# Performance work log

Hardware: AMD Instinct MI355X
Metric: run time of the kernel (lower is better)

## Reference

```python
import jax, jax.numpy as jnp
import numpy as np

H, W, L = 512, 512, 28
N_ITER = 12
SIGMA = 0.5
LAM = 1.0
PI = 3.141592653589793


def _offsets(s, phi_deg):
    # Matches torch: dx = s*cos(phi), dy = s*sin(phi), shifted to min 0, round-half-even.
    phi = phi_deg * PI / 180.0
    dx = s * np.cos(phi)
    dy = s * np.sin(phi)
    dx = dx - dx.min()
    dy = dy - dy.min()
    return np.rint(dx).astype(np.int32), np.rint(dy).astype(np.int32)


def _gauss_kernel(sigma):
    ksize = max(3, int(6 * sigma + 1) | 1)  # 5 for sigma=0.5
    ax = np.arange(ksize, dtype=np.float32) - ksize // 2
    g1 = np.exp(-0.5 * (ax / sigma) ** 2)
    g1 = g1 / g1.sum()
    g2 = np.outer(g1, g1).astype(np.float32)
    return jnp.asarray(g2)[None, None], ksize // 2  # [1,1,k,k], pad


def setup_inputs():
    k1, k2 = jax.random.split(jax.random.key(0))
    s_nom = jnp.arange(L, dtype=jnp.float32)
    phi_d_deg = jnp.ones((), dtype=jnp.float32)
    dx, dy = _offsets(np.arange(L, dtype=np.float32), 1.0)
    Hp, Wp = H + int(dy.max()), W + int(dx.max())
    y_1hw = jax.random.uniform(k1, (1, Hp, Wp), dtype=jnp.float32)
    mask2d = jax.random.uniform(k2, (H, W), dtype=jnp.float32)
    return {"y_1hw": y_1hw, "mask2d": mask2d, "phi_d_deg": phi_d_deg, "s_nom": s_nom}


def reference(y_1hw, mask2d, phi_d_deg, s_nom):
    # Integer dispersion offsets are detached (.item()) in the original, so they
    # are compile-time constants here.
    dx, dy = _offsets(np.asarray(s_nom), float(np.asarray(phi_d_deg)))
    Hp, Wp = H + int(dy.max()), W + int(dx.max())
    rows = dy[:, None, None] + np.arange(H, dtype=np.int64)[None, :, None]  # [L,H,1]
    cols = dx[:, None, None] + np.arange(W, dtype=np.int64)[None, None, :]  # [L,1,W]
    flat = jnp.asarray(rows * Wp + cols)  # [L,H,W] flat indices into [Hp*Wp]

    g2, pad = _gauss_kernel(SIGMA)

    def A(x):  # CASSI forward: [L,H,W] -> [Hp,Wp] batched scatter-add
        return jnp.zeros(Hp * Wp, x.dtype).at[flat].add(mask2d[None] * x).reshape(Hp, Wp)

    def At(y2):  # CASSI adjoint: [Hp,Wp] -> [L,H,W] batched gather
        return y2.reshape(-1)[flat] * mask2d[None]

    def denoise(x):  # depthwise 5x5 Gaussian; same 2D kernel per band -> bands as batch
        return jax.lax.conv_general_dilated(
            x[:, None], g2, (1, 1), [(pad, pad), (pad, pad)])[:, 0]

    # Phi_sum = sum over bands of shifted mask, clamped to >= 1
    Phi_sum = jnp.maximum(
        jnp.zeros(Hp * Wp, mask2d.dtype).at[flat].add(
            jnp.broadcast_to(mask2d[None], (L, H, W))).reshape(Hp, Wp),
        1.0)

    y = y_1hw[0]
    x = At(y)   # adjoint back-projection initialization
    y1 = y
    for _ in range(N_ITER):  # unrolled GAP iterations (accelerated GAP)
        yb = A(x)
        y1 = y1 + (y - yb)
        x = x + LAM * At((y1 - yb) / Phi_sum)
        x = denoise(x)
    return x[None]  # [1, L, H, W]
```

## Files before the change

kernel.cpp:

```cpp
#include <hip/hip_runtime.h>

#define HH 512
#define WW 512
#define LL 28
#define WP 539
#define NPIX (HH * WP)
#define NX (LL * HH * WW)

#define TX 64
#define TY 16
#define GB 7
#define NGRP (LL / GB)

__global__ void k_setup(const float* __restrict__ y, const float* __restrict__ mask,
                        float* __restrict__ phi_inv, float* __restrict__ y1) {
    int idx = blockIdx.x * blockDim.x + threadIdx.x;
    if (idx >= NPIX) return;
    int i = idx / WP, jp = idx - i * WP;
    int lmin = jp - (WW - 1); if (lmin < 0) lmin = 0;
    int lmax = jp < (LL - 1) ? jp : (LL - 1);
    float s = 0.f;
    for (int l = lmin; l <= lmax; ++l) s += mask[i * WW + (jp - l)];
    phi_inv[idx] = 1.0f / fmaxf(s, 1.0f);
    y1[idx] = y[idx];
}

__global__ void k_xinit(const float* __restrict__ y, const float* __restrict__ mask,
                        float* __restrict__ x, float* __restrict__ yb) {
    __shared__ float ybl[TY][TX + GB - 1];
    const int l0 = blockIdx.z * GB;
    const int bi = blockIdx.y * TY;
    const int bj = blockIdx.x * TX;
    const int tid = threadIdx.x;

    for (int idx = tid; idx < TY * (TX + GB - 1); idx += 256)
        ybl[idx / (TX + GB - 1)][idx % (TX + GB - 1)] = 0.f;
    __syncthreads();

    for (int l = l0; l < l0 + GB; ++l) {
        #pragma unroll
        for (int k = 0; k < 4; ++k) {
            int idx = tid + k * 256;
            int r = idx / TX, c = idx - r * TX;
            int gi = bi + r, gj = bj + c;
            float m = mask[gi * WW + gj];
            float v = y[gi * WP + gj + l] * m;
            x[((size_t)l * HH + gi) * WW + gj] = v;
            ybl[r][c + (l - l0)] += m * v;
        }
        __syncthreads();
    }
    for (int idx = tid; idx < TY * (TX + GB - 1); idx += 256) {
        int r = idx / (TX + GB - 1), c = idx % (TX + GB - 1);
        atomicAdd(&yb[(bi + r) * WP + bj + l0 + c], ybl[r][c]);
    }
}

__global__ void k_pix(const float* __restrict__ y, const float* __restrict__ phi_inv,
                      float* __restrict__ y1, float* __restrict__ t, float* __restrict__ yb) {
    int idx = blockIdx.x * blockDim.x + threadIdx.x;
    if (idx >= NPIX / 4) return;
    float4 ybv = ((const float4*)yb)[idx];
    float4 yv  = ((const float4*)y)[idx];
    float4 y1v = ((const float4*)y1)[idx];
    float4 pv  = ((const float4*)phi_inv)[idx];
    float4 y1n, tv;
    y1n.x = y1v.x + yv.x - ybv.x;  tv.x = (y1n.x - ybv.x) * pv.x;
    y1n.y = y1v.y + yv.y - ybv.y;  tv.y = (y1n.y - ybv.y) * pv.y;
    y1n.z = y1v.z + yv.z - ybv.z;  tv.z = (y1n.z - ybv.z) * pv.z;
    y1n.w = y1v.w + yv.w - ybv.w;  tv.w = (y1n.w - ybv.w) * pv.w;
    ((float4*)y1)[idx] = y1n;
    ((float4*)t)[idx]  = tv;
    ((float4*)yb)[idx] = make_float4(0.f, 0.f, 0.f, 0.f);
}

template <bool LAST>
__global__ void k_iter(const float* __restrict__ x, const float* __restrict__ t,
                       const float* __restrict__ mask, float* __restrict__ xo,
                       float* __restrict__ yb, float w0, float w1, float w2) {
    __shared__ float msk[TY + 4][TX + 4];
    __shared__ float u[TY + 4][TX + 4];
    __shared__ float hb[TY + 4][TX];
    __shared__ float ybl[TY][TX + GB - 1];

    const int l0 = blockIdx.z * GB;
    const int bi = blockIdx.y * TY;
    const int bj = blockIdx.x * TX;
    const int tid = threadIdx.x;

    for (int idx = tid; idx < (TY + 4) * (TX + 4); idx += 256) {
        int r = idx / (TX + 4), c = idx - r * (TX + 4);
        int gi = bi + r - 2, gj = bj + c - 2;
        msk[r][c] = (gi >= 0 && gi < HH && gj >= 0 && gj < WW) ? mask[gi * WW + gj] : 0.f;
    }
    if (!LAST)
        for (int idx = tid; idx < TY * (TX + GB - 1); idx += 256)
            ybl[idx / (TX + GB - 1)][idx % (TX + GB - 1)] = 0.f;
    __syncthreads();

    for (int l = l0; l < l0 + GB; ++l) {
        const float* xl = x + (size_t)l * HH * WW;
        for (int idx = tid; idx < (TY + 4) * (TX + 4); idx += 256) {
            int r = idx / (TX + 4), c = idx - r * (TX + 4);
            int gi = bi + r - 2, gj = bj + c - 2;
            float v = 0.f;
            if (gi >= 0 && gi < HH && gj >= 0 && gj < WW)
                v = xl[gi * WW + gj] + t[gi * WP + gj + l] * msk[r][c];
            u[r][c] = v;
        }
        __syncthreads();
        for (int idx = tid; idx < (TY + 4) * TX; idx += 256) {
            int r = idx / TX, c = idx - r * TX;
            hb[r][c] = w2 * (u[r][c] + u[r][c + 4])
                     + w1 * (u[r][c + 1] + u[r][c + 3])
                     + w0 * u[r][c + 2];
        }
        __syncthreads();
        #pragma unroll
        for (int k = 0; k < 4; ++k) {
            int idx = tid + k * 256;
            int r = idx / TX, c = idx - r * TX;
            float o = w2 * (hb[r][c] + hb[r + 4][c])
                    + w1 * (hb[r + 1][c] + hb[r + 3][c])
                    + w0 * hb[r + 2][c];
            xo[((size_t)l * HH + bi + r) * WW + bj + c] = o;
            if (!LAST) ybl[r][c + (l - l0)] += msk[r + 2][c + 2] * o;
        }
        __syncthreads();
    }

    if (!LAST)
        for (int idx = tid; idx < TY * (TX + GB - 1); idx += 256) {
            int r = idx / (TX + GB - 1), c = idx % (TX + GB - 1);
            atomicAdd(&yb[(bi + r) * WP + bj + l0 + c], ybl[r][c]);
        }
}

extern "C" void kernel_launch(void* const* d_in, const int* in_sizes, int n_in,
                              void* d_out, int out_size, void* d_ws, size_t ws_size,
                              hipStream_t stream) {
    const float* y    = (const float*)d_in[0];
    const float* mask = (const float*)d_in[1];

    float* out = (float*)d_out;

    float* phi_inv = (float*)d_ws;
    float* y1      = phi_inv + NPIX;
    float* t       = y1 + NPIX;
    float* yb      = t + NPIX;
    float* xA      = yb + NPIX;
    float* xB      = out;

    float g1 = expf(-2.0f), g2 = expf(-8.0f);
    float gs = 1.0f + 2.0f * g1 + 2.0f * g2;
    float w0 = 1.0f / gs, w1 = g1 / gs, w2 = g2 / gs;

    const int BT = 256;
    const dim3 tgrid(WW / TX, HH / TY, NGRP);

    hipMemsetAsync(yb, 0, NPIX * sizeof(float), stream);
    k_setup<<<(NPIX + BT - 1) / BT, BT, 0, stream>>>(y, mask, phi_inv, y1);
    k_xinit<<<tgrid, BT, 0, stream>>>(y, mask, xB, yb);

    float* cur = xB;
    float* nxt = xA;
    for (int it = 0; it < 12; ++it) {
        k_pix<<<(NPIX / 4 + BT - 1) / BT, BT, 0, stream>>>(y, phi_inv, y1, t, yb);
        if (it < 11)
            k_iter<false><<<tgrid, BT, 0, stream>>>(cur, t, mask, nxt, yb, w0, w1, w2);
        else
            k_iter<true><<<tgrid, BT, 0, stream>>>(cur, t, mask, nxt, yb, w0, w1, w2);
        float* tmp = cur; cur = nxt; nxt = tmp;
    }
}
```

Before: 484.1 us.

## Stage t tile once per band group in LDS and simplify tile indexing

Loads the shifted t halo tile once per block into shared memory, covering all bands in the group, instead of re-reading t from global memory for every band. It replaces the div/mod index loops with fixed 2D thread mapping (tx,ty) and a separate bounds-check-free fast path for interior tiles. It also adds launch bounds and uses fma. This cuts global traffic and integer overhead at the cost of extra LDS usage and more code.

Result: slower. 550.1 us (+13.6%).

```diff
diff --git a/kernel.cpp b/kernel.cpp
--- a/kernel.cpp
+++ b/kernel.cpp
@@ -25,38 +25,45 @@
     y1[idx] = y[idx];
 }
 
-__global__ void k_xinit(const float* __restrict__ y, const float* __restrict__ mask,
+__global__ __launch_bounds__(256) void k_xinit(const float* __restrict__ y, const float* __restrict__ mask,
                         float* __restrict__ x, float* __restrict__ yb) {
     __shared__ float ybl[TY][TX + GB - 1];
     const int l0 = blockIdx.z * GB;
     const int bi = blockIdx.y * TY;
     const int bj = blockIdx.x * TX;
     const int tid = threadIdx.x;
-
-    for (int idx = tid; idx < TY * (TX + GB - 1); idx += 256)
-        ybl[idx / (TX + GB - 1)][idx % (TX + GB - 1)] = 0.f;
+    const int tx = tid & 63;
+    const int ty = tid >> 6;
+
+    #pragma unroll
+    for (int k = 0; k < 4; ++k) {
+        int r = ty + 4 * k;
+        ybl[r][tx] = 0.f;
+        if (tx < GB - 1) ybl[r][64 + tx] = 0.f;
+    }
     __syncthreads();
 
     for (int l = l0; l < l0 + GB; ++l) {
         #pragma unroll
         for (int k = 0; k < 4; ++k) {
-            int idx = tid + k * 256;
-            int r = idx / TX, c = idx - r * TX;
-            int gi = bi + r, gj = bj + c;
+            int r = ty + 4 * k;
+            int gi = bi + r, gj = bj + tx;
             float m = mask[gi * WW + gj];
             float v = y[gi * WP + gj + l] * m;
             x[((size_t)l * HH + gi) * WW + gj] = v;
-            ybl[r][c + (l - l0)] += m * v;
-        }
-        __syncthreads();
-    }
-    for (int idx = tid; idx < TY * (TX + GB - 1); idx += 256) {
-        int r = idx / (TX + GB - 1), c = idx % (TX + GB - 1);
-        atomicAdd(&yb[(bi + r) * WP + bj + l0 + c], ybl[r][c]);
-    }
-}
-
-__global__ void k_pix(const float* __restrict__ y, const float* __restrict__ phi_inv,
+            ybl[r][tx + (l - l0)] += m * v;
+        }
+        __syncthreads();
+    }
+    #pragma unroll
+    for (int k = 0; k < 4; ++k) {
+        int r = ty + 4 * k;
+        atomicAdd(&yb[(bi + r) * WP + bj + l0 + tx], ybl[r][tx]);
+        if (tx < GB - 1) atomicAdd(&yb[(bi + r) * WP + bj + l0 + 64 + tx], ybl[r][64 + tx]);
+    }
+}
+
+__global__ __launch_bounds__(256) void k_pix(const float* __restrict__ y, const float* __restrict__ phi_inv,
                       float* __restrict__ y1, float* __restrict__ t, float* __restrict__ yb) {
     int idx = blockIdx.x * blockDim.x + threadIdx.x;
     if (idx >= NPIX / 4) return;
@@ -75,10 +82,11 @@
 }
 
 template <bool LAST>
-__global__ void k_iter(const float* __restrict__ x, const float* __restrict__ t,
+__global__ __launch_bounds__(256) void k_iter(const float* __restrict__ x, const float* __restrict__ t,
                        const float* __restrict__ mask, float* __restrict__ xo,
                        float* __restrict__ yb, float w0, float w1, float w2) {
     __shared__ float msk[TY + 4][TX + 4];
+    __shared__ float tld[TY + 4][TX + 4 + GB - 1];
     __shared__ float u[TY + 4][TX + 4];
     __shared__ float hb[TY + 4][TX];
     __shared__ float ybl[TY][TX + GB - 1];
@@ -87,53 +95,106 @@
     const int bi = blockIdx.y * TY;
     const int bj = blockIdx.x * TX;
     const int tid = threadIdx.x;
-
-    for (int idx = tid; idx < (TY + 4) * (TX + 4); idx += 256) {
-        int r = idx / (TX + 4), c = idx - r * (TX + 4);
-        int gi = bi + r - 2, gj = bj + c - 2;
-        msk[r][c] = (gi >= 0 && gi < HH && gj >= 0 && gj < WW) ? mask[gi * WW + gj] : 0.f;
-    }
-    if (!LAST)
-        for (int idx = tid; idx < TY * (TX + GB - 1); idx += 256)
-            ybl[idx / (TX + GB - 1)][idx % (TX + GB - 1)] = 0.f;
+    const int tx = tid & 63;
+    const int ty = tid >> 6;
+    const bool edge = (bi == 0) | (bi == HH - TY) | (bj == 0) | (bj == WW - TX);
+
+    #pragma unroll
+    for (int k = 0; k < 5; ++k) {
+        int r = ty + 4 * k;
+        int gi = bi + r - 2;
+        bool rok = (gi >= 0) & (gi < HH);
+        int gj0 = bj + tx - 2;
+        float m0 = 0.f;
+        if (rok & (gj0 >= 0) & (gj0 < WW)) m0 = mask[gi * WW + gj0];
+        msk[r][tx] = m0;
+        if (tx < 4) {
+            int gj1 = bj + 64 + tx - 2;
+            float m1 = 0.f;
+            if (rok & (gj1 < WW)) m1 = mask[gi * WW + gj1];
+            msk[r][64 + tx] = m1;
+        }
+        int tg0 = bj - 2 + l0 + tx;
+        float v0 = 0.f;
+        if (rok & (tg0 >= 0) & (tg0 < WP)) v0 = t[gi * WP + tg0];
+        tld[r][tx] = v0;
+        if (tx < 4 + GB - 1) {
+            int tg1 = tg0 + 64;
+            float v1 = 0.f;
+            if (rok & (tg1 < WP)) v1 = t[gi * WP + tg1];
+            tld[r][64 + tx] = v1;
+        }
+    }
+    if (!LAST) {
+        #pragma unroll
+        for (int k = 0; k < 4; ++k) {
+            int r = ty + 4 * k;
+            ybl[r][tx] = 0.f;
+            if (tx < GB - 1) ybl[r][64 + tx] = 0.f;
+        }
+    }
     __syncthreads();
 
     for (int l = l0; l < l0 + GB; ++l) {
         const float* xl = x + (size_t)l * HH * WW;
-        for (int idx = tid; idx < (TY + 4) * (TX + 4); idx += 256) {
-            int r = idx / (TX + 4), c = idx - r * (TX + 4);
-            int gi = bi + r - 2, gj = bj + c - 2;
-            float v = 0.f;
-            if (gi >= 0 && gi < HH && gj >= 0 && gj < WW)
-                v = xl[gi * WW + gj] + t[gi * WP + gj + l] * msk[r][c];
-            u[r][c] = v;
-        }
-        __syncthreads();
-        for (int idx = tid; idx < (TY + 4) * TX; idx += 256) {
-            int r = idx / TX, c = idx - r * TX;
-            hb[r][c] = w2 * (u[r][c] + u[r][c + 4])
-                     + w1 * (u[r][c + 1] + u[r][c + 3])
-                     + w0 * u[r][c + 2];
-        }
-        __syncthreads();
-        #pragma unroll
-        for (int k = 0; k < 4; ++k) {
-            int idx = tid + k * 256;
-            int r = idx / TX, c = idx - r * TX;
-            float o = w2 * (hb[r][c] + hb[r + 4][c])
-                    + w1 * (hb[r + 1][c] + hb[r + 3][c])
-                    + w0 * hb[r + 2][c];
-            xo[((size_t)l * HH + bi + r) * WW + bj + c] = o;
-            if (!LAST) ybl[r][c + (l - l0)] += msk[r + 2][c + 2] * o;
-        }
-        __syncthreads();
-    }
-
-    if (!LAST)
-        for (int idx = tid; idx < TY * (TX + GB - 1); idx += 256) {
-            int r = idx / (TX + GB - 1), c = idx % (TX + GB - 1);
-            atomicAdd(&yb[(bi + r) * WP + bj + l0 + c], ybl[r][c]);
-        }
+        const int dl = l - l0;
+        if (!edge) {
+            #pragma unroll
+            for (int k = 0; k < 5; ++k) {
+                int r = ty + 4 * k;
+                const float* xrow = xl + (bi + r - 2) * WW + bj - 2;
+                u[r][tx] = fmaf(tld[r][tx + dl], msk[r][tx], xrow[tx]);
+                if (tx < 4) u[r][64 + tx] = fmaf(tld[r][64 + tx + dl], msk[r][64 + tx], xrow[64 + tx]);
+            }
+        } else {
+            #pragma unroll
+            for (int k = 0; k < 5; ++k) {
+                int r = ty + 4 * k;
+                int gi = bi + r - 2;
+                bool rok = (gi >= 0) & (gi < HH);
+                int gj0 = bj + tx - 2;
+                float v0 = 0.f;
+                if (rok & (gj0 >= 0) & (gj0 < WW))
+                    v0 = fmaf(tld[r][tx + dl], msk[r][tx], xl[gi * WW + gj0]);
+                u[r][tx] = v0;
+                if (tx < 4) {
+                    int gj1 = bj + 64 + tx - 2;
+                    float v1 = 0.f;
+                    if (rok & (gj1 < WW))
+                        v1 = fmaf(tld[r][64 + tx + dl], msk[r][64 + tx], xl[gi * WW + gj1]);
+                    u[r][64 + tx] = v1;
+                }
+            }
+        }
+        __syncthreads();
+        #pragma unroll
+        for (int k = 0; k < 5; ++k) {
+            int r = ty + 4 * k;
+            hb[r][tx] = w2 * (u[r][tx] + u[r][tx + 4])
+                      + w1 * (u[r][tx + 1] + u[r][tx + 3])
+                      + w0 * u[r][tx + 2];
+        }
+        __syncthreads();
+        #pragma unroll
+        for (int k = 0; k < 4; ++k) {
+            int r = ty + 4 * k;
+            float o = w2 * (hb[r][tx] + hb[r + 4][tx])
+                    + w1 * (hb[r + 1][tx] + hb[r + 3][tx])
+                    + w0 * hb[r + 2][tx];
+            xo[((size_t)l * HH + bi + r) * WW + bj + tx] = o;
+            if (!LAST) ybl[r][tx + dl] += msk[r + 2][tx + 2] * o;
+        }
+        __syncthreads();
+    }
+
+    if (!LAST) {
+        #pragma unroll
+        for (int k = 0; k < 4; ++k) {
+            int r = ty + 4 * k;
+            atomicAdd(&yb[(bi + r) * WP + bj + l0 + tx], ybl[r][tx]);
+            if (tx < GB - 1) atomicAdd(&yb[(bi + r) * WP + bj + l0 + 64 + tx], ybl[r][64 + tx]);
+        }
+    }
 }
 
 extern "C" void kernel_launch(void* const* d_in, const int* in_sizes, int n_in,
```
